# Performance work log

Hardware: AMD Instinct MI355X
Metric: run time of the kernel (lower is better)

Reference implementation:

```python
import jax, jax.numpy as jnp
import numpy as np

NODE_SIZE = 128
EDGE_SIZE = 20
CUTOFF = 5.0
N_NODES = 20000
N_EDGES = 600000


def silu(x):
    return x * jax.nn.sigmoid(x)


def setup_inputs() -> dict:
    key = jax.random.key(0)
    ks = jax.random.split(key, 20)
    d = NODE_SIZE
    inp = {
        "node_states_scalar": jax.random.normal(ks[0], (N_NODES, d), jnp.float32),
        "node_states_vector": jax.random.normal(ks[1], (N_NODES, 3, d), jnp.float32),
        "edge_states": jax.random.normal(ks[2], (N_EDGES, EDGE_SIZE), jnp.float32),
        "edge_vectors": jax.random.normal(ks[3], (N_EDGES, 3), jnp.float32),
        "edge_norms": jax.random.uniform(ks[4], (N_EDGES, 1), jnp.float32),
        "edge_index": jax.random.randint(ks[5], (N_EDGES, 2), 0, N_NODES, jnp.int64 if jax.config.jax_enable_x64 else jnp.int32),
        # parameters, stored as [in, out] so y = x @ W + b
        "Wf": jax.random.normal(ks[6], (EDGE_SIZE, 3 * d), jnp.float32) * 0.05,
        "bf": jnp.zeros((3 * d,), jnp.float32),
        "Wm1": jax.random.normal(ks[7], (d, d), jnp.float32) * 0.05,
        "bm1": jnp.zeros((d,), jnp.float32),
        "Wm2": jax.random.normal(ks[8], (d, 3 * d), jnp.float32) * 0.05,
        "bm2": jnp.zeros((3 * d,), jnp.float32),
        "WU": jax.random.normal(ks[9], (d, d), jnp.float32) * 0.05,
        "WV": jax.random.normal(ks[10], (d, d), jnp.float32) * 0.05,
        "Wa1": jax.random.normal(ks[11], (2 * d, d), jnp.float32) * 0.05,
        "ba1": jnp.zeros((d,), jnp.float32),
        "Wa2": jax.random.normal(ks[12], (d, 3 * d), jnp.float32) * 0.05,
        "ba2": jnp.zeros((3 * d,), jnp.float32),
    }
    return inp


def reference(node_states_scalar, node_states_vector, edge_states, edge_vectors,
              edge_norms, edge_index, Wf, bf, Wm1, bm1, Wm2, bm2, WU, WV,
              Wa1, ba1, Wa2, ba2):
    d = NODE_SIZE
    n = node_states_scalar.shape[0]

    # --- message function ---
    # cosine cutoff: 0.5*(cos(pi*r/cutoff)+1) for r < cutoff, else 0
    fc = 0.5 * (jnp.cos(jnp.pi * edge_norms / CUTOFF) + 1.0)
    fc = jnp.where(edge_norms < CUTOFF, fc, 0.0)                      # [E,1]
    filter_weight = (edge_states @ Wf + bf) * fc                      # [E,3d]
    scalar_output = silu(node_states_scalar @ Wm1 + bm1) @ Wm2 + bm2  # [N,3d]

    src = edge_index[:, 0]
    dst = edge_index[:, 1]
    filter_output = filter_weight * scalar_output[src]                # [E,3d]
    gate_nodes = filter_output[:, :d]
    gate_edges = filter_output[:, d:2 * d]
    messages_scalar = filter_output[:, 2 * d:]

    gated_node_vec = node_states_vector[src] * gate_nodes[:, None, :]     # [E,3,d]
    gated_edge_vec = gate_edges[:, None, :] * edge_vectors[:, :, None]    # [E,3,d]
    messages_vector = gated_node_vec + gated_edge_vec

    ds_m = jax.ops.segment_sum(messages_scalar, dst, num_segments=n)  # [N,d]
    dv_m = jax.ops.segment_sum(messages_vector, dst, num_segments=n)  # [N,3,d]

    s = node_states_scalar + ds_m
    v = node_states_vector + dv_m

    # --- node state update ---
    Uv = jnp.einsum('nvd,de->nve', v, WU)
    Vv = jnp.einsum('nvd,de->nve', v, WV)
    Vv_sq = jnp.sum(Vv ** 2, axis=1)                                  # [N,d]
    a = silu(jnp.concatenate([s, Vv_sq], axis=1) @ Wa1 + ba1) @ Wa2 + ba2
    a_ss, a_sv, a_vv = a[:, :d], a[:, d:2 * d], a[:, 2 * d:]
    ip = jnp.sum(Uv * Vv, axis=1)                                     # [N,d]

    s = s + a_ss + a_sv * ip
    v = v + a_vv[:, None, :] * Uv
    return (s, v)
```

## Files before the change

### kernel.cpp

```cpp
#include <hip/hip_runtime.h>

#define ND 128
#define ESZ 20
#define NN 20000
#define NE 600000
#define PI_F 3.14159265358979323846f
#define CUT 5.0f

using short8 = __attribute__((ext_vector_type(8))) short;
using f32x4  = __attribute__((ext_vector_type(4))) float;
using hh2    = __attribute__((ext_vector_type(2))) _Float16;

__device__ __forceinline__ float silu_f(float x) { return x / (1.0f + __expf(-x)); }

__device__ __forceinline__ unsigned short f2bf(float x) {
    unsigned u = __float_as_uint(x);
    unsigned r = (u + 0x7FFFu + ((u >> 16) & 1u)) >> 16;
    return (unsigned short)r;
}
__device__ __forceinline__ float bf2f(unsigned short h) {
    return __uint_as_float(((unsigned)h) << 16);
}
__device__ __forceinline__ unsigned pack2h(float x, float y) {
    _Float16 a = (_Float16)x, b = (_Float16)y;
    unsigned short ua = __builtin_bit_cast(unsigned short, a);
    unsigned short ub = __builtin_bit_cast(unsigned short, b);
    return (unsigned)ua | ((unsigned)ub << 16);
}
__device__ __forceinline__ float dot2u(unsigned a, hh2 b, float acc) {
    return __builtin_amdgcn_fdot2(__builtin_bit_cast(hh2, a), b, acc, false);
}

__device__ __forceinline__ void pack_w(const float* __restrict__ W,
                                       unsigned short* __restrict__ P,
                                       int s, int K, int N) {
    int k = s / N, n = s - k * N;
    int dst = ((((n >> 4) * (K >> 5) + (k >> 5)) * 64) +
               (((k >> 3) & 3) << 4) + (n & 15)) * 8 + (k & 7);
    P[dst] = f2bf(W[s]);
}

#define R0 1920000L
#define R1 (R0 + 180224L)
#define R2 (R1 + 4224L)
#define R3 (R2 + 600000L)

__global__ __launch_bounds__(256) void k_front(
    const float4* __restrict__ ns4, const float4* __restrict__ nsv4,
    const int* __restrict__ eidx,
    const float* __restrict__ Wf, const float* __restrict__ bfb,
    const float* __restrict__ Wm1, const float* __restrict__ Wm2,
    const float* __restrict__ WU, const float* __restrict__ WV,
    const float* __restrict__ Wa1, const float* __restrict__ Wa2,
    float4* __restrict__ outs4, float4* __restrict__ outv4,
    ushort4* __restrict__ nsb4, unsigned* __restrict__ gnh,
    unsigned short* __restrict__ p1, unsigned short* __restrict__ p2,
    unsigned short* __restrict__ pU, unsigned short* __restrict__ pV,
    unsigned short* __restrict__ pa1, unsigned short* __restrict__ pa2,
    unsigned* __restrict__ wfh, int* __restrict__ counts) {
    long gid = (long)blockIdx.x * 256 + threadIdx.x;
    if (gid < R0) {
        long i = gid;
        const long S4 = (long)NN * ND / 4;
        if (i < S4) {
            float4 v = ns4[i];
            outs4[i] = v;
            ushort4 h; h.x = f2bf(v.x); h.y = f2bf(v.y); h.z = f2bf(v.z); h.w = f2bf(v.w);
            nsb4[i] = h;
        }
        float4 w = nsv4[i];
        outv4[i] = w;
        unsigned short* gs = (unsigned short*)gnh;
        long b = i * 4;
        gs[(b + 0) * 2 + 1] = f2bf(w.x);
        gs[(b + 1) * 2 + 1] = f2bf(w.y);
        gs[(b + 2) * 2 + 1] = f2bf(w.z);
        gs[(b + 3) * 2 + 1] = f2bf(w.w);
    } else if (gid < R1) {
        int i = (int)(gid - R0);
        if      (i <  16384) pack_w(Wm1, p1, i,          128, 128);
        else if (i <  65536) pack_w(Wm2, p2, i - 16384,  128, 384);
        else if (i <  81920) pack_w(WU,  pU, i - 65536,  128, 128);
        else if (i <  98304) pack_w(WV,  pV, i - 81920,  128, 128);
        else if (i < 131072) pack_w(Wa1, pa1, i - 98304, 256, 128);
        else                 pack_w(Wa2, pa2, i - 131072,128, 384);
    } else if (gid < R2) {
        int j = (int)(gid - R1);
        int p = j / 384, cc = j - p * 384;
        float a = 0.f, b = 0.f;
        if (p < 10) { a = Wf[(2 * p) * 384 + cc]; b = Wf[(2 * p + 1) * 384 + cc]; }
        else if (p == 10) { a = bfb[cc]; }
        wfh[p * 384 + cc] = pack2h(a, b);
    } else if (gid < R3) {
        int e = (int)(gid - R2);
        atomicAdd(&counts[eidx[2 * e + 1]], 1);
    }
}

#define SCAN_T 1024
__global__ __launch_bounds__(SCAN_T) void k_scan(const int* __restrict__ counts,
                                                 int* __restrict__ offsets,
                                                 int* __restrict__ cursor) {
    __shared__ int part[SCAN_T];
    const int t = threadIdx.x;
    const int CPT = (NN + SCAN_T - 1) / SCAN_T;
    const int base = t * CPT;
    int sum = 0;
    for (int i = 0; i < CPT; ++i) {
        int idx = base + i;
        if (idx < NN) sum += counts[idx];
    }
    part[t] = sum;
    __syncthreads();
    for (int off = 1; off < SCAN_T; off <<= 1) {
        int v = (t >= off) ? part[t - off] : 0;
        __syncthreads();
        part[t] += v;
        __syncthreads();
    }
    int run = (t == 0) ? 0 : part[t - 1];
    for (int i = 0; i < CPT; ++i) {
        int idx = base + i;
        if (idx < NN) {
            offsets[idx] = run;
            cursor[idx] = run;
            run += counts[idx];
        }
    }
    if (t == SCAN_T - 1) offsets[NN] = run;
}

#define SCAT_B 2344
__global__ __launch_bounds__(256) void k_sm(
    const int* __restrict__ eidx, int* __restrict__ cursor,
    const float* __restrict__ es, const float* __restrict__ enorm,
    const float* __restrict__ evec, unsigned* __restrict__ rec,
    const unsigned short* __restrict__ nsb,
    const unsigned short* __restrict__ Wm1p, const float* __restrict__ bm1,
    const unsigned short* __restrict__ Wm2p, const float* __restrict__ bm2,
    unsigned* __restrict__ gnh) {
    __shared__ unsigned short lsh[4][16][136];
    if (blockIdx.x < SCAT_B) {
        int e = blockIdx.x * 256 + threadIdx.x;
        if (e < NE) {
            int s  = eidx[2 * e];
            int dd = eidx[2 * e + 1];
            float nrm = enorm[e];
            float fc = (nrm < CUT) ? 0.5f * (__cosf(PI_F * nrm * (1.0f / CUT)) + 1.0f) : 0.0f;
            const float* er = es + (long)e * ESZ;
            unsigned qv[11];
#pragma unroll
            for (int p = 0; p < 10; ++p)
                qv[p] = pack2h(er[2 * p] * fc, er[2 * p + 1] * fc);
            qv[10] = pack2h(fc, 0.f);
            float e0 = evec[3 * e + 0], e1 = evec[3 * e + 1], e2 = evec[3 * e + 2];
            int pos = atomicAdd(&cursor[dd], 1);
            uint4* rp = (uint4*)rec + (long)pos * 4;
            rp[0] = make_uint4((unsigned)s, (unsigned)dd,
                               __float_as_uint(e0), __float_as_uint(e1));
            rp[1] = make_uint4(__float_as_uint(e2), qv[0], qv[1], qv[2]);
            rp[2] = make_uint4(qv[3], qv[4], qv[5], qv[6]);
            rp[3] = make_uint4(qv[7], qv[8], qv[9], qv[10]);
        }
        return;
    }
    const int lane = threadIdx.x & 63;
    const int wv = threadIdx.x >> 6;
    const int wid = (blockIdx.x - SCAT_B) * 4 + wv;
    const int m0 = wid * 16;
    if (m0 >= NN) return;
    const int ml = lane & 15, q = lane >> 4;

    short8 a1[4];
#pragma unroll
    for (int kb = 0; kb < 4; ++kb)
        a1[kb] = *(const short8*)(nsb + (long)(m0 + ml) * ND + kb * 32 + q * 8);

#pragma unroll
    for (int nt = 0; nt < 8; ++nt) {
        float b = bm1[nt * 16 + ml];
        f32x4 acc = {b, b, b, b};
#pragma unroll
        for (int kb = 0; kb < 4; ++kb) {
            short8 bf = *(const short8*)(Wm1p + ((nt * 4 + kb) * 64 + lane) * 8);
            acc = __builtin_amdgcn_mfma_f32_16x16x32_bf16(a1[kb], bf, acc, 0, 0, 0);
        }
#pragma unroll
        for (int r = 0; r < 4; ++r)
            lsh[wv][q * 4 + r][nt * 16 + ml] = f2bf(silu_f(acc[r]));
    }
    __syncthreads();

    short8 a2[4];
#pragma unroll
    for (int kb = 0; kb < 4; ++kb)
        a2[kb] = *(const short8*)(&lsh[wv][ml][kb * 32 + q * 8]);

    unsigned short* gs = (unsigned short*)gnh;
#pragma unroll
    for (int nt = 0; nt < 24; ++nt) {
        float b = bm2[nt * 16 + ml];
        f32x4 acc = {b, b, b, b};
#pragma unroll
        for (int kb = 0; kb < 4; ++kb) {
            short8 bf = *(const short8*)(Wm2p + ((nt * 4 + kb) * 64 + lane) * 8);
            acc = __builtin_amdgcn_mfma_f32_16x16x32_bf16(a2[kb], bf, acc, 0, 0, 0);
        }
#pragma unroll
        for (int r = 0; r < 4; ++r) {
            long idx = (long)(m0 + q * 4 + r) * 384 + nt * 16 + ml;
            gs[idx * 2] = f2bf(acc[r]);
        }
    }
}

#define NGRP 8192
#define RUN ((NE + NGRP - 1) / NGRP)

#define SL(R, k) { R = *(const uint4*)(rec + ((long)beg + (long)(k) * 16) * 16 + lane * 4); }
#define SW(R, k) { *(uint4*)&eb[wv][(k) & 1][lane * 4] = R; }

#define LREAD(S, l_) {                                                        \
    int ll = ((l_) < nl) ? (l_) : nl - 1;                                     \
    const unsigned* ep_ = &eb[wv][(ll >> 4) & 1][(ll & 15) << 4];             \
    m0##S = *(const uint4*)(ep_);                                             \
    m1##S = *(const uint4*)(ep_ + 4);                                         \
    m2##S = *(const uint4*)(ep_ + 8);                                         \
    m3##S = *(const uint4*)(ep_ + 12);                                        \
}

#define LGATH(S) {                                                            \
    int s_ = __builtin_amdgcn_readfirstlane((int)m0##S.x);                    \
    dst##S = __builtin_amdgcn_readfirstlane((int)m0##S.y);                    \
    const unsigned* gp_ = gnh + (long)s_ * 384;                               \
    x0##S = gp_[t]; x1##S = gp_[128 + t]; x2##S = gp_[256 + t];               \
}

#define FLUSH() {                                                             \
    atomicAdd(&out_s[(long)cur_dst * ND + t], as);                            \
    atomicAdd(&out_v[(long)cur_dst * 384 + 0 * ND + t], av0);                 \
    atomicAdd(&out_v[(long)cur_dst * 384 + 1 * ND + t], av1);                 \
    atomicAdd(&out_v[(long)cur_dst * 384 + 2 * ND + t], av2);                 \
}

#define COMPE(S) {                                                            \
    if (dst##S != cur_dst) {                                                  \
        if (cur_dst >= 0) FLUSH();                                            \
        cur_dst = dst##S;                                                     \
        as = 0.f; av0 = 0.f; av1 = 0.f; av2 = 0.f;                            \
    }                                                                         \
    unsigned ea_[11] = {m1##S.y, m1##S.z, m1##S.w,                            \
                        m2##S.x, m2##S.y, m2##S.z, m2##S.w,                   \
                        m3##S.x, m3##S.y, m3##S.z, m3##S.w};                  \
    float f0 = 0.f, f1 = 0.f, f2 = 0.f;                                       \
    _Pragma("unroll")                                                         \
    for (int p = 0; p < 11; ++p) {                                            \
        f0 = dot2u(ea_[p], wf[p][0], f0);                                     \
        f1 = dot2u(ea_[p], wf[p][1], f1);                                     \
        f2 = dot2u(ea_[p], wf[p][2], f2);                                     \
    }                                                                         \
    f0 *= __uint_as_float(x0##S << 16);                                       \
    f1 *= __uint_as_float(x1##S << 16);                                       \
    f2 *= __uint_as_float(x2##S << 16);                                       \
    float ev0_ = __uint_as_float(m0##S.z);                                    \
    float ev1_ = __uint_as_float(m0##S.w);                                    \
    float ev2_ = __uint_as_float(m1##S.x);                                    \
    as  += f2;                                                                \
    av0 += __uint_as_float(x0##S & 0xffff0000u) * f0 + f1 * ev0_;             \
    av1 += __uint_as_float(x1##S & 0xffff0000u) * f0 + f1 * ev1_;             \
    av2 += __uint_as_float(x2##S & 0xffff0000u) * f0 + f1 * ev2_;             \
}

__global__ __launch_bounds__(256, 4) void k_edge6(
    const unsigned* __restrict__ rec, const unsigned* __restrict__ wfh,
    const unsigned* __restrict__ gnh,
    float* __restrict__ out_s, float* __restrict__ out_v) {
    __shared__ __align__(16) unsigned eb[4][2][256];
    const int wv = threadIdx.x >> 6;
    const int lane = threadIdx.x & 63;
    const int grp = blockIdx.x * 2 + (wv >> 1);
    const int t = ((wv & 1) << 6) | lane;
    const int beg = grp * RUN;
    const int end = (beg + RUN < NE) ? beg + RUN : NE;
    if (beg >= end) return;
    const int nl = end - beg;

    hh2 wf[11][3];
#pragma unroll
    for (int p = 0; p < 11; ++p)
#pragma unroll
        for (int c = 0; c < 3; ++c)
            wf[p][c] = __builtin_bit_cast(hh2, wfh[p * 384 + c * 128 + t]);

    uint4 st0, st1;
    uint4 m0A, m1A, m2A, m3A, m0B, m1B, m2B, m3B;
    unsigned x0A, x1A, x2A, x0B, x1B, x2B;
    int dstA, dstB;

    SL(st0, 0); SL(st1, 1);
    SW(st0, 0); SW(st1, 1);
    SL(st0, 2);

    LREAD(A, 0); LGATH(A);
    LREAD(B, 1); LGATH(B);

    int cur_dst = -1;
    float as = 0.f, av0 = 0.f, av1 = 0.f, av2 = 0.f;

    for (int l = 0; l < nl; l += 2) {
        if (l && !(l & 15)) {
            int c = l >> 4;
            if ((c + 1) & 1) { SW(st1, c + 1); SL(st0, c + 2); }
            else             { SW(st0, c + 1); SL(st1, c + 2); }
        }
        COMPE(A);
        LREAD(A, l + 2);
        COMPE(B);
        LGATH(A);
        LREAD(B, l + 3);
        LGATH(B);
    }
    FLUSH();
}

__global__ __launch_bounds__(256) void k_uvm(
    const float* __restrict__ out_v, const float* __restrict__ out_s,
    const unsigned short* __restrict__ WUp, const unsigned short* __restrict__ WVp,
    unsigned short* __restrict__ Uvh, unsigned short* __restrict__ cat,
    float* __restrict__ ipb) {
    const int lane = threadIdx.x & 63;
    const int wid = blockIdx.x * 4 + (threadIdx.x >> 6);
    const int m0 = wid * 16;
    if (m0 >= NN) return;
    const int ml = lane & 15, q = lane >> 4;

#pragma unroll
    for (int j = 0; j < 32; ++j) {
        int idx = j * 64 + lane;
        int n = m0 + (idx >> 7), c = idx & 127;
        cat[(long)n * 256 + c] = f2bf(out_s[(long)n * 128 + c]);
    }

    short8 av[3][4];
#pragma unroll
    for (int ax = 0; ax < 3; ++ax)
#pragma unroll
        for (int kb = 0; kb < 4; ++kb) {
            const float* p = out_v + (long)(m0 + ml) * 384 + ax * 128 + kb * 32 + q * 8;
            float4 x = *(const float4*)p;
            float4 y = *(const float4*)(p + 4);
            short8 s;
            s[0] = (short)f2bf(x.x); s[1] = (short)f2bf(x.y);
            s[2] = (short)f2bf(x.z); s[3] = (short)f2bf(x.w);
            s[4] = (short)f2bf(y.x); s[5] = (short)f2bf(y.y);
            s[6] = (short)f2bf(y.z); s[7] = (short)f2bf(y.w);
            av[ax][kb] = s;
        }

#pragma unroll
    for (int nt = 0; nt < 8; ++nt) {
        f32x4 u0 = {0.f,0.f,0.f,0.f}, u1 = u0, u2 = u0;
        f32x4 v0 = u0, v1 = u0, v2 = u0;
#pragma unroll
        for (int kb = 0; kb < 4; ++kb) {
            short8 bu = *(const short8*)(WUp + ((nt * 4 + kb) * 64 + lane) * 8);
            short8 bv = *(const short8*)(WVp + ((nt * 4 + kb) * 64 + lane) * 8);
            u0 = __builtin_amdgcn_mfma_f32_16x16x32_bf16(av[0][kb], bu, u0, 0, 0, 0);
            u1 = __builtin_amdgcn_mfma_f32_16x16x32_bf16(av[1][kb], bu, u1, 0, 0, 0);
            u2 = __builtin_amdgcn_mfma_f32_16x16x32_bf16(av[2][kb], bu, u2, 0, 0, 0);
            v0 = __builtin_amdgcn_mfma_f32_16x16x32_bf16(av[0][kb], bv, v0, 0, 0, 0);
            v1 = __builtin_amdgcn_mfma_f32_16x16x32_bf16(av[1][kb], bv, v1, 0, 0, 0);
            v2 = __builtin_amdgcn_mfma_f32_16x16x32_bf16(av[2][kb], bv, v2, 0, 0, 0);
        }
        const int c = nt * 16 + ml;
#pragma unroll
        for (int r = 0; r < 4; ++r) {
            long grow = m0 + q * 4 + r;
            float vs  = v0[r] * v0[r] + v1[r] * v1[r] + v2[r] * v2[r];
            float ipv = u0[r] * v0[r] + u1[r] * v1[r] + u2[r] * v2[r];
            cat[grow * 256 + 128 + c] = f2bf(vs);
            ipb[grow * 128 + c] = ipv;
            Uvh[(grow * 3 + 0) * 128 + c] = f2bf(u0[r]);
            Uvh[(grow * 3 + 1) * 128 + c] = f2bf(u1[r]);
            Uvh[(grow * 3 + 2) * 128 + c] = f2bf(u2[r]);
        }
    }
}

__global__ __launch_bounds__(256) void k_att(
    const unsigned short* __restrict__ cat,
    const unsigned short* __restrict__ Wa1p, const float* __restrict__ ba1,
    const unsigned short* __restrict__ Wa2p, const float* __restrict__ ba2,
    const float* __restrict__ ipb, const unsigned short* __restrict__ Uvh,
    float* __restrict__ out_s, float* __restrict__ out_v) {
    const int lane = threadIdx.x & 63;
    const int wv = threadIdx.x >> 6;
    const int wid = blockIdx.x * 4 + wv;
    const int m0 = wid * 16;
    if (m0 >= NN) return;
    const int ml = lane & 15, q = lane >> 4;
    __shared__ unsigned short lsh[4][16][136];

    short8 a1[8];
#pragma unroll
    for (int kb = 0; kb < 8; ++kb)
        a1[kb] = *(const short8*)(cat + (long)(m0 + ml) * 256 + kb * 32 + q * 8);

#pragma unroll
    for (int nt = 0; nt < 8; ++nt) {
        float b = ba1[nt * 16 + ml];
        f32x4 acc = {b, b, b, b};
#pragma unroll
        for (int kb = 0; kb < 8; ++kb) {
            short8 bf = *(const short8*)(Wa1p + ((nt * 8 + kb) * 64 + lane) * 8);
            acc = __builtin_amdgcn_mfma_f32_16x16x32_bf16(a1[kb], bf, acc, 0, 0, 0);
        }
#pragma unroll
        for (int r = 0; r < 4; ++r)
            lsh[wv][q * 4 + r][nt * 16 + ml] = f2bf(silu_f(acc[r]));
    }
    __syncthreads();

    short8 h[4];
#pragma unroll
    for (int kb = 0; kb < 4; ++kb)
        h[kb] = *(const short8*)(&lsh[wv][ml][kb * 32 + q * 8]);

#pragma unroll
    for (int nt = 0; nt < 8; ++nt) {
        float b0 = ba2[nt * 16 + ml];
        float b1 = ba2[128 + nt * 16 + ml];
        f32x4 aS = {b0, b0, b0, b0};
        f32x4 aG = {b1, b1, b1, b1};
#pragma unroll
        for (int kb = 0; kb < 4; ++kb) {
            short8 bS = *(const short8*)(Wa2p + (((nt) * 4 + kb) * 64 + lane) * 8);
            short8 bG = *(const short8*)(Wa2p + (((nt + 8) * 4 + kb) * 64 + lane) * 8);
            aS = __builtin_amdgcn_mfma_f32_16x16x32_bf16(h[kb], bS, aS, 0, 0, 0);
            aG = __builtin_amdgcn_mfma_f32_16x16x32_bf16(h[kb], bG, aG, 0, 0, 0);
        }
#pragma unroll
        for (int r = 0; r < 4; ++r) {
            long grow = m0 + q * 4 + r;
            long o = grow * 128 + nt * 16 + ml;
            float ipv = ipb[o];
            out_s[o] = out_s[o] + aS[r] + aG[r] * ipv;
        }
    }

#pragma unroll
    for (int nt = 0; nt < 8; ++nt) {
        float b2 = ba2[256 + nt * 16 + ml];
        f32x4 aV = {b2, b2, b2, b2};
#pragma unroll
        for (int kb = 0; kb < 4; ++kb) {
            short8 bV = *(const short8*)(Wa2p + (((nt + 16) * 4 + kb) * 64 + lane) * 8);
            aV = __builtin_amdgcn_mfma_f32_16x16x32_bf16(h[kb], bV, aV, 0, 0, 0);
        }
#pragma unroll
        for (int r = 0; r < 4; ++r) {
            long grow = m0 + q * 4 + r;
            int c = nt * 16 + ml;
#pragma unroll
            for (int ax = 0; ax < 3; ++ax) {
                float u = bf2f(Uvh[(grow * 3 + ax) * 128 + c]);
                long o = grow * 384 + ax * 128 + c;
                out_v[o] = out_v[o] + aV[r] * u;
            }
        }
    }
}

extern "C" void kernel_launch(void* const* d_in, const int* in_sizes, int n_in,
                              void* d_out, int out_size, void* d_ws, size_t ws_size,
                              hipStream_t stream) {
    const float* ns    = (const float*)d_in[0];
    const float* nsv   = (const float*)d_in[1];
    const float* es    = (const float*)d_in[2];
    const float* evec  = (const float*)d_in[3];
    const float* enorm = (const float*)d_in[4];
    const int*   eidx  = (const int*)d_in[5];
    const float* Wf    = (const float*)d_in[6];
    const float* bfb   = (const float*)d_in[7];
    const float* Wm1   = (const float*)d_in[8];
    const float* bm1   = (const float*)d_in[9];
    const float* Wm2   = (const float*)d_in[10];
    const float* bm2   = (const float*)d_in[11];
    const float* WU    = (const float*)d_in[12];
    const float* WV    = (const float*)d_in[13];
    const float* Wa1   = (const float*)d_in[14];
    const float* ba1   = (const float*)d_in[15];
    const float* Wa2   = (const float*)d_in[16];
    const float* ba2   = (const float*)d_in[17];

    float* out_s = (float*)d_out;
    float* out_v = out_s + (size_t)NN * ND;

    char* w = (char*)d_ws;
    unsigned short* p1  = (unsigned short*)(w + 0);
    unsigned short* p2  = (unsigned short*)(w + 32768);
    unsigned short* pU  = (unsigned short*)(w + 131072);
    unsigned short* pV  = (unsigned short*)(w + 163840);
    unsigned short* pa1 = (unsigned short*)(w + 196608);
    unsigned short* pa2 = (unsigned short*)(w + 262144);
    unsigned* wfh = (unsigned*)(w + 360448);
    int* counts = (int*)(w + 377344);
    int* offs   = (int*)(w + 457344);
    int* cursor = (int*)(w + 537408);
    unsigned* rec = (unsigned*)(w + 617408);
    char* u0 = w + 39024576;
    unsigned* gnh       = (unsigned*)(u0);
    unsigned short* nsb = (unsigned short*)(u0 + 30720000);
    unsigned short* Uvh = (unsigned short*)(u0);
    unsigned short* cat = (unsigned short*)(u0 + 15360000);
    float*          ipb = (float*)(u0 + 25600000);

    hipMemsetAsync(counts, 0, (size_t)NN * sizeof(int), stream);
    k_front<<<(int)((R3 + 255) / 256), 256, 0, stream>>>(
        (const float4*)ns, (const float4*)nsv, eidx, Wf, bfb,
        Wm1, Wm2, WU, WV, Wa1, Wa2,
        (float4*)out_s, (float4*)out_v, (ushort4*)nsb, gnh,
        p1, p2, pU, pV, pa1, pa2, wfh, counts);
    k_scan<<<1, SCAN_T, 0, stream>>>(counts, offs, cursor);
    k_sm<<<SCAT_B + 313, 256, 0, stream>>>(eidx, cursor, es, enorm, evec, rec,
                                           nsb, p1, bm1, p2, bm2, gnh);
    k_edge6<<<NGRP / 2, 256, 0, stream>>>(rec, wfh, gnh, out_s, out_v);
    k_uvm<<<313, 256, 0, stream>>>(out_v, out_s, pU, pV, Uvh, cat, ipb);
    k_att<<<313, 256, 0, stream>>>(cat, pa1, ba1, pa2, ba2, ipb, Uvh,
                                   out_s, out_v);
}
```

Baseline: 529.4 us.

## Deepen gather prefetch in edge kernel with fixed 80-edge runs and readlane indices

Replaces the edge aggregation kernel with a version that processes fixed 80-edge runs in 16-edge chunks, reading per-chunk src/dst once and broadcasting via readlane. Node-feature gathers are issued eight edges ahead in a register ring instead of two, aiming to hide global gather latency. Tail records are zero-padded with a memset so chunk over-reads are safe. Increases register use and lowers occupancy bound to 3.

```diff
diff --git a/kernel.cpp b/kernel.cpp
--- a/kernel.cpp
+++ b/kernel.cpp
@@ -214,27 +214,8 @@
     }
 }
 
-#define NGRP 8192
-#define RUN ((NE + NGRP - 1) / NGRP)
-
-#define SL(R, k) { R = *(const uint4*)(rec + ((long)beg + (long)(k) * 16) * 16 + lane * 4); }
-#define SW(R, k) { *(uint4*)&eb[wv][(k) & 1][lane * 4] = R; }
-
-#define LREAD(S, l_) {                                                        \
-    int ll = ((l_) < nl) ? (l_) : nl - 1;                                     \
-    const unsigned* ep_ = &eb[wv][(ll >> 4) & 1][(ll & 15) << 4];             \
-    m0##S = *(const uint4*)(ep_);                                             \
-    m1##S = *(const uint4*)(ep_ + 4);                                         \
-    m2##S = *(const uint4*)(ep_ + 8);                                         \
-    m3##S = *(const uint4*)(ep_ + 12);                                        \
-}
-
-#define LGATH(S) {                                                            \
-    int s_ = __builtin_amdgcn_readfirstlane((int)m0##S.x);                    \
-    dst##S = __builtin_amdgcn_readfirstlane((int)m0##S.y);                    \
-    const unsigned* gp_ = gnh + (long)s_ * 384;                               \
-    x0##S = gp_[t]; x1##S = gp_[128 + t]; x2##S = gp_[256 + t];               \
-}
+#define NGRP 7500
+#define RUN 80
 
 #define FLUSH() {                                                             \
     atomicAdd(&out_s[(long)cur_dst * ND + t], as);                            \
@@ -243,15 +224,29 @@
     atomicAdd(&out_v[(long)cur_dst * 384 + 2 * ND + t], av2);                 \
 }
 
-#define COMPE(S) {                                                            \
-    if (dst##S != cur_dst) {                                                  \
+#define STEP(k, dk, gsrc) {                                                   \
+    if (dk != cur_dst) {                                                      \
         if (cur_dst >= 0) FLUSH();                                            \
-        cur_dst = dst##S;                                                     \
+        cur_dst = dk;                                                         \
         as = 0.f; av0 = 0.f; av1 = 0.f; av2 = 0.f;                            \
     }                                                                         \
-    unsigned ea_[11] = {m1##S.y, m1##S.z, m1##S.w,                            \
-                        m2##S.x, m2##S.y, m2##S.z, m2##S.w,                   \
-                        m3##S.x, m3##S.y, m3##S.z, m3##S.w};                  \
+    const uint4 M0_ = pp[(k) & 1][0], M1_ = pp[(k) & 1][1],                   \
+                M2_ = pp[(k) & 1][2], M3_ = pp[(k) & 1][3];                   \
+    const unsigned XA_ = xr[(k) & 7][0], XB_ = xr[(k) & 7][1],                \
+                   XC_ = xr[(k) & 7][2];                                      \
+                                            \
+    { const unsigned* pb_ = (((k) + 2 < 16) ? bc : bn) + ((((k) + 2) & 15) << 4); \
+      pp[(k) & 1][0] = *(const uint4*)(pb_);                                  \
+      pp[(k) & 1][1] = *(const uint4*)(pb_ + 4);                              \
+      pp[(k) & 1][2] = *(const uint4*)(pb_ + 8);                              \
+      pp[(k) & 1][3] = *(const uint4*)(pb_ + 12); }                           \
+                                                         \
+    { const unsigned* gp_ = gnh + (long)(gsrc) * 384;                         \
+      xr[(k) & 7][0] = gp_[t];                                                \
+      xr[(k) & 7][1] = gp_[128 + t];                                          \
+      xr[(k) & 7][2] = gp_[256 + t]; }                                        \
+    unsigned ea_[11] = {M1_.y, M1_.z, M1_.w, M2_.x, M2_.y, M2_.z, M2_.w,      \
+                        M3_.x, M3_.y, M3_.z, M3_.w};                          \
     float f0 = 0.f, f1 = 0.f, f2 = 0.f;                                       \
     _Pragma("unroll")                                                         \
     for (int p = 0; p < 11; ++p) {                                            \
@@ -259,19 +254,18 @@
         f1 = dot2u(ea_[p], wf[p][1], f1);                                     \
         f2 = dot2u(ea_[p], wf[p][2], f2);                                     \
     }                                                                         \
-    f0 *= __uint_as_float(x0##S << 16);                                       \
-    f1 *= __uint_as_float(x1##S << 16);                                       \
-    f2 *= __uint_as_float(x2##S << 16);                                       \
-    float ev0_ = __uint_as_float(m0##S.z);                                    \
-    float ev1_ = __uint_as_float(m0##S.w);                                    \
-    float ev2_ = __uint_as_float(m1##S.x);                                    \
+    f0 *= __uint_as_float(XA_ << 16);                                         \
+    f1 *= __uint_as_float(XB_ << 16);                                         \
+    f2 *= __uint_as_float(XC_ << 16);                                         \
     as  += f2;                                                                \
-    av0 += __uint_as_float(x0##S & 0xffff0000u) * f0 + f1 * ev0_;             \
-    av1 += __uint_as_float(x1##S & 0xffff0000u) * f0 + f1 * ev1_;             \
-    av2 += __uint_as_float(x2##S & 0xffff0000u) * f0 + f1 * ev2_;             \
-}
-
-__global__ __launch_bounds__(256, 4) void k_edge6(
+    av0 += __uint_as_float(XA_ & 0xffff0000u) * f0 + f1 * __uint_as_float(M0_.z); \
+    av1 += __uint_as_float(XB_ & 0xffff0000u) * f0 + f1 * __uint_as_float(M0_.w); \
+    av2 += __uint_as_float(XC_ & 0xffff0000u) * f0 + f1 * __uint_as_float(M1_.x); \
+}
+
+#define RL(v, j) __builtin_amdgcn_readlane((int)(v), (j))
+
+__global__ __launch_bounds__(256, 3) void k_edge7(
     const unsigned* __restrict__ rec, const unsigned* __restrict__ wfh,
     const unsigned* __restrict__ gnh,
     float* __restrict__ out_s, float* __restrict__ out_v) {
@@ -280,10 +274,7 @@
     const int lane = threadIdx.x & 63;
     const int grp = blockIdx.x * 2 + (wv >> 1);
     const int t = ((wv & 1) << 6) | lane;
-    const int beg = grp * RUN;
-    const int end = (beg + RUN < NE) ? beg + RUN : NE;
-    if (beg >= end) return;
-    const int nl = end - beg;
+    const long beg = (long)grp * RUN;
 
     hh2 wf[11][3];
 #pragma unroll
@@ -292,33 +283,68 @@
         for (int c = 0; c < 3; ++c)
             wf[p][c] = __builtin_bit_cast(hh2, wfh[p * 384 + c * 128 + t]);
 
-    uint4 st0, st1;
-    uint4 m0A, m1A, m2A, m3A, m0B, m1B, m2B, m3B;
-    unsigned x0A, x1A, x2A, x0B, x1B, x2B;
-    int dstA, dstB;
-
-    SL(st0, 0); SL(st1, 1);
-    SW(st0, 0); SW(st1, 1);
-    SL(st0, 2);
-
-    LREAD(A, 0); LGATH(A);
-    LREAD(B, 1); LGATH(B);
+    unsigned* const b0 = &eb[wv][0][0];
+    unsigned* const b1 = &eb[wv][1][0];
+
+    uint4 sA = *(const uint4*)(rec + (beg + 0)  * 16 + lane * 4);
+    uint4 sB = *(const uint4*)(rec + (beg + 16) * 16 + lane * 4);
+    uint4 st = *(const uint4*)(rec + (beg + 32) * 16 + lane * 4);
+    *(uint4*)&b0[lane * 4] = sA;
+    *(uint4*)&b1[lane * 4] = sB;
+    uint2 sdC = *(const uint2*)&b0[(lane & 15) << 4];
+    uint2 sdN = *(const uint2*)&b1[(lane & 15) << 4];
+
+    uint4 pp[2][4];
+    pp[0][0] = *(const uint4*)(b0 + 0);  pp[0][1] = *(const uint4*)(b0 + 4);
+    pp[0][2] = *(const uint4*)(b0 + 8);  pp[0][3] = *(const uint4*)(b0 + 12);
+    pp[1][0] = *(const uint4*)(b0 + 16); pp[1][1] = *(const uint4*)(b0 + 20);
+    pp[1][2] = *(const uint4*)(b0 + 24); pp[1][3] = *(const uint4*)(b0 + 28);
+
+    unsigned xr[8][3];
+#define IG(j) { int s_ = RL(sdC.x, j);                                        \
+                const unsigned* gp_ = gnh + (long)s_ * 384;                   \
+                xr[j][0] = gp_[t]; xr[j][1] = gp_[128 + t];                   \
+                xr[j][2] = gp_[256 + t]; }
+    IG(0) IG(1) IG(2) IG(3) IG(4) IG(5) IG(6) IG(7)
+#undef IG
 
     int cur_dst = -1;
     float as = 0.f, av0 = 0.f, av1 = 0.f, av2 = 0.f;
 
-    for (int l = 0; l < nl; l += 2) {
-        if (l && !(l & 15)) {
-            int c = l >> 4;
-            if ((c + 1) & 1) { SW(st1, c + 1); SL(st0, c + 2); }
-            else             { SW(st0, c + 1); SL(st1, c + 2); }
-        }
-        COMPE(A);
-        LREAD(A, l + 2);
-        COMPE(B);
-        LGATH(A);
-        LREAD(B, l + 3);
-        LGATH(B);
+    for (int c = 0; c < 5; ++c) {
+        unsigned* const bc = &eb[wv][c & 1][0];
+        unsigned* const bn = &eb[wv][(c + 1) & 1][0];
+        const int d0  = RL(sdC.y, 0),  d1  = RL(sdC.y, 1);
+        const int d2  = RL(sdC.y, 2),  d3  = RL(sdC.y, 3);
+        const int d4  = RL(sdC.y, 4),  d5  = RL(sdC.y, 5);
+        const int d6  = RL(sdC.y, 6),  d7  = RL(sdC.y, 7);
+        const int d8  = RL(sdC.y, 8),  d9  = RL(sdC.y, 9);
+        const int d10 = RL(sdC.y, 10), d11 = RL(sdC.y, 11);
+        const int d12 = RL(sdC.y, 12), d13 = RL(sdC.y, 13);
+        const int d14 = RL(sdC.y, 14), d15 = RL(sdC.y, 15);
+        const int s8  = RL(sdC.x, 8),  s9  = RL(sdC.x, 9);
+        const int s10 = RL(sdC.x, 10), s11 = RL(sdC.x, 11);
+        const int s12 = RL(sdC.x, 12), s13 = RL(sdC.x, 13);
+        const int s14 = RL(sdC.x, 14), s15 = RL(sdC.x, 15);
+
+        STEP(0, d0, s8)   STEP(1, d1, s9)   STEP(2, d2, s10)  STEP(3, d3, s11)
+        STEP(4, d4, s12)  STEP(5, d5, s13)  STEP(6, d6, s14)  STEP(7, d7, s15)
+
+        const int gm = (c < 4) ? -1 : 0;
+        const int n0 = RL(sdN.x, 0) & gm, n1 = RL(sdN.x, 1) & gm;
+        const int n2 = RL(sdN.x, 2) & gm, n3 = RL(sdN.x, 3) & gm;
+        const int n4 = RL(sdN.x, 4) & gm, n5 = RL(sdN.x, 5) & gm;
+        const int n6 = RL(sdN.x, 6) & gm, n7 = RL(sdN.x, 7) & gm;
+
+        STEP(8,  d8,  n0)  STEP(9,  d9,  n1)  STEP(10, d10, n2) STEP(11, d11, n3)
+        STEP(12, d12, n4)  STEP(13, d13, n5)  STEP(14, d14, n6) STEP(15, d15, n7)
+
+        if (c < 4) {
+            *(uint4*)&bc[lane * 4] = st;
+            st = *(const uint4*)(rec + (beg + (long)(c + 3) * 16) * 16 + lane * 4);
+            sdC = sdN;
+            sdN = *(const uint2*)&bc[(lane & 15) << 4];
+        }
     }
     FLUSH();
 }
@@ -516,6 +542,7 @@
     float*          ipb = (float*)(u0 + 25600000);
 
     hipMemsetAsync(counts, 0, (size_t)NN * sizeof(int), stream);
+    hipMemsetAsync(rec + (size_t)NE * 16, 0, 112 * 64, stream);
     k_front<<<(int)((R3 + 255) / 256), 256, 0, stream>>>(
         (const float4*)ns, (const float4*)nsv, eidx, Wf, bfb,
         Wm1, Wm2, WU, WV, Wa1, Wa2,
@@ -524,7 +551,7 @@
     k_scan<<<1, SCAN_T, 0, stream>>>(counts, offs, cursor);
     k_sm<<<SCAT_B + 313, 256, 0, stream>>>(eidx, cursor, es, enorm, evec, rec,
                                            nsb, p1, bm1, p2, bm2, gnh);
-    k_edge6<<<NGRP / 2, 256, 0, stream>>>(rec, wfh, gnh, out_s, out_v);
+    k_edge7<<<NGRP / 2, 256, 0, stream>>>(rec, wfh, gnh, out_s, out_v);
     k_uvm<<<313, 256, 0, stream>>>(out_v, out_s, pU, pV, Uvh, cat, ipb);
     k_att<<<313, 256, 0, stream>>>(cat, pa1, ba1, pa2, ba2, ipb, Uvh,
                                    out_s, out_v);
```

Result: faster. 517.4 us (-2.3%).
